# Kernel optimization log

Hardware: AMD Instinct MI355X
Metric: run time of the kernel (lower is better)

The kernel has to match this reference:

```python
import jax, jax.numpy as jnp
import numpy as np

N_ENT = 200000; N_USR = 100000; D = 64
E = 1500000; NI = 1000000
HOPS = 2; N_ITER = 3; N_VIRT = 3; N_REL = 11
EPS = 1e-12


def setup_inputs() -> dict:
    key = jax.random.key(0)
    ks = jax.random.split(key, 8)
    entity_emb = jax.random.normal(ks[0], (N_ENT, D), jnp.float32) * 0.1
    user_emb = jax.random.normal(ks[1], (N_USR, D), jnp.float32) * 0.1
    latent_emb = jax.random.normal(ks[2], (N_VIRT, D), jnp.float32)
    rel_weight = jax.random.normal(ks[3], (N_REL - 1, D), jnp.float32)
    # per-hop Aggregator.w, initialized as in the module
    agg_w = jnp.tile(jnp.array([0.4, 0.3, 0.3], jnp.float32), (HOPS, 1))
    edge_index = jax.random.randint(ks[4], (2, E), 0, N_ENT)
    edge_type = jax.random.randint(ks[5], (E,), 1, N_REL)  # values in [1, n_relations-1]
    user_index = jax.random.randint(ks[6], (NI,), 0, N_USR)
    item_index = jax.random.randint(ks[7], (NI,), 0, N_ENT)
    return dict(entity_emb=entity_emb, user_emb=user_emb, latent_emb=latent_emb,
                rel_weight=rel_weight, agg_w=agg_w, edge_index=edge_index,
                edge_type=edge_type, user_index=user_index, item_index=item_index)


def _l2norm(x):
    n = jnp.linalg.norm(x, axis=1, keepdims=True)
    return x / jnp.maximum(n, EPS)


def _squash(u):
    sq = jnp.sum(u * u, axis=1, keepdims=True)  # ||u||^2
    return (sq / (sq + 1.0)) * _l2norm(u)


def _lws_entity(entity_emb, head, tail, mask_f):
    """LWS over a single virtual-relation edge subset (mask_f zeroes other edges).
    Matches torch: neigh is cumulatively sim-scaled across iterations."""
    cnt = jax.ops.segment_sum(mask_f, head, num_segments=N_ENT)
    denom = jnp.maximum(cnt, 1.0)[:, None]
    neigh = entity_emb[tail] * mask_f[:, None]          # [E, D]
    u = None
    for it in range(N_ITER):
        if u is not None:
            sim = jnp.sum(u[head] * neigh, axis=1, keepdims=True)
            neigh = sim * neigh
        u = jax.ops.segment_sum(neigh, head, num_segments=N_ENT) / denom
        if it < N_ITER - 1:
            u = _squash(u)
        u = u + entity_emb
    return u


def _lws_user(entity_emb, user_emb, user_index, item_index):
    """LWS for users; neigh is re-gathered fresh each iteration (as in torch)."""
    ones = jnp.ones((item_index.shape[0],), entity_emb.dtype)
    cnt = jax.ops.segment_sum(ones, user_index, num_segments=N_USR)
    denom = jnp.maximum(cnt, 1.0)[:, None]
    u = None
    for it in range(N_ITER):
        neigh = entity_emb[item_index]                  # [NI, D]
        if u is not None:
            sim = jnp.sum(u[user_index] * neigh, axis=1, keepdims=True)
            neigh = sim * neigh
        u = jax.ops.segment_sum(neigh, user_index, num_segments=N_USR) / denom
        if it < N_ITER - 1:
            u = _squash(u)
        u = u + user_emb
    return u


def reference(entity_emb, user_emb, latent_emb, rel_weight, agg_w,
              edge_index, edge_type, user_index, item_index):
    head, tail = edge_index[0], edge_index[1]
    # relation -> virtual-relation routing (argmax over similarity)
    relation_remap = jnp.argmax(rel_weight @ latent_emb.T, axis=1)   # [n_rel-1]
    et = relation_remap[edge_type - 1]                               # [E] in [0, N_VIRT)

    entity_res = entity_emb
    user_res = user_emb
    ent = entity_emb
    usr = user_emb
    for hop in range(HOPS):
        items = [_lws_entity(ent, head, tail, (et == i).astype(ent.dtype))
                 for i in range(N_VIRT)]
        w = jax.nn.softmax(agg_w[hop])                               # [3]
        entity_agg = w[0] * items[0] + w[1] * items[1] + w[2] * items[2]
        user_agg = _lws_user(ent, usr, user_index, item_index)
        # no dropout (eval mode); normalize + residual
        ent = _l2norm(entity_agg)
        usr = _l2norm(user_agg)
        entity_res = entity_res + ent
        user_res = user_res + usr
    return jnp.concatenate([entity_res, user_res], axis=0)          # [N_ENT+N_USR, D]
```

## Files before the change

### kernel.cpp

```cpp
#include <hip/hip_runtime.h>

#define N_ENT 200000
#define N_USR 100000
#define NT3   700000
#define UKEY0 600000
#define DIM 64
#define NE 1500000
#define NI_ 1000000
#define NTE 2500000
#define NREL1 10
#define NVIRT 3
#define EPSF 1e-12f
#define SCAN_B 1024
#define RE 6
#define RU 12

__device__ __forceinline__ float4 f4_zero() { return make_float4(0.f, 0.f, 0.f, 0.f); }
__device__ __forceinline__ float4 f4_add(float4 a, float4 b) {
    return make_float4(a.x + b.x, a.y + b.y, a.z + b.z, a.w + b.w);
}
__device__ __forceinline__ float4 f4_scale(float s, float4 a) {
    return make_float4(s * a.x, s * a.y, s * a.z, s * a.w);
}
__device__ __forceinline__ float4 f4_fma(float s, float4 a, float4 b) {
    return make_float4(fmaf(s, a.x, b.x), fmaf(s, a.y, b.y), fmaf(s, a.z, b.z), fmaf(s, a.w, b.w));
}
__device__ __forceinline__ float f4_dot(float4 a, float4 b) {
    return a.x * b.x + a.y * b.y + a.z * b.z + a.w * b.w;
}

__device__ __forceinline__ float red16(float v) {
    int x;
    x = __builtin_amdgcn_update_dpp(0, __float_as_int(v), 0xB1, 0xF, 0xF, true);
    v += __int_as_float(x);
    x = __builtin_amdgcn_update_dpp(0, __float_as_int(v), 0x4E, 0xF, 0xF, true);
    v += __int_as_float(x);
    x = __builtin_amdgcn_update_dpp(0, __float_as_int(v), 0x124, 0xF, 0xF, true);
    v += __int_as_float(x);
    x = __builtin_amdgcn_update_dpp(0, __float_as_int(v), 0x128, 0xF, 0xF, true);
    v += __int_as_float(x);
    return v;
}

__device__ __forceinline__ float4 squash4(float4 u, float sq) {
    float n = sqrtf(sq);
    float s = sq / ((sq + 1.f) * fmaxf(n, EPSF));
    return f4_scale(s, u);
}

__global__ void k_prep(const float* __restrict__ rw, const float* __restrict__ lat,
                       const float* __restrict__ aw, int* __restrict__ remap,
                       float* __restrict__ wsoft) {
    int t = threadIdx.x;
    if (t < NREL1) {
        float best = -3.4e38f; int bi = 0;
        for (int j = 0; j < NVIRT; j++) {
            float s = 0.f;
            for (int d = 0; d < DIM; d++) s += rw[t * DIM + d] * lat[j * DIM + d];
            if (s > best) { best = s; bi = j; }
        }
        remap[t] = bi;
    }
    if (t >= 32 && t < 34) {
        int h = t - 32;
        float a0 = aw[h * 3 + 0], a1 = aw[h * 3 + 1], a2 = aw[h * 3 + 2];
        float m = fmaxf(a0, fmaxf(a1, a2));
        float e0 = expf(a0 - m), e1 = expf(a1 - m), e2 = expf(a2 - m);
        float s = e0 + e1 + e2;
        wsoft[h * 3 + 0] = e0 / s; wsoft[h * 3 + 1] = e1 / s; wsoft[h * 3 + 2] = e2 / s;
    }
}

__global__ void k_count_all(const int* __restrict__ head, const int* __restrict__ etype,
                            const int* __restrict__ remap, const int* __restrict__ uidx,
                            int* __restrict__ cnt) {
    int i = blockIdx.x * blockDim.x + threadIdx.x;
    if (i < NE) {
        int key = head[i] * 3 + remap[etype[i] - 1];
        atomicAdd(&cnt[key], 1);
    } else if (i < NTE) {
        atomicAdd(&cnt[UKEY0 + uidx[i - NE]], 1);
    }
}

__global__ void k_scan1(const int* __restrict__ in, int* __restrict__ excl,
                        int* __restrict__ bsum, int n) {
    __shared__ int s[SCAN_B];
    int tid = threadIdx.x, gid = blockIdx.x * SCAN_B + tid;
    int v = (gid < n) ? in[gid] : 0;
    s[tid] = v; __syncthreads();
    for (int off = 1; off < SCAN_B; off <<= 1) {
        int t = 0;
        if (tid >= off) t = s[tid - off];
        __syncthreads();
        s[tid] += t;
        __syncthreads();
    }
    if (gid < n) excl[gid] = s[tid] - v;
    if (tid == SCAN_B - 1) bsum[blockIdx.x] = s[tid];
}

__global__ void k_scan2(int* __restrict__ bsum, int nb) {
    __shared__ int s[SCAN_B];
    int tid = threadIdx.x;
    int v = (tid < nb) ? bsum[tid] : 0;
    s[tid] = v; __syncthreads();
    for (int off = 1; off < SCAN_B; off <<= 1) {
        int t = 0;
        if (tid >= off) t = s[tid - off];
        __syncthreads();
        s[tid] += t;
        __syncthreads();
    }
    if (tid < nb) bsum[tid] = s[tid] - v;
}

__global__ void k_scan3(const int* __restrict__ excl, const int* __restrict__ bsum,
                        const int* __restrict__ cnt, int* __restrict__ rp,
                        int* __restrict__ cur, int n) {
    int gid = blockIdx.x * SCAN_B + threadIdx.x;
    if (gid < n) {
        int v = excl[gid] + bsum[blockIdx.x];
        rp[gid] = v;
        cur[gid] = v;
        if (gid == n - 1) rp[n] = v + cnt[gid];
    }
}

__global__ void k_scatter_all(const int* __restrict__ head, const int* __restrict__ tail,
                              const int* __restrict__ etype, const int* __restrict__ remap,
                              const int* __restrict__ uidx, const int* __restrict__ iidx,
                              int* __restrict__ cur, int* __restrict__ sorted) {
    int i = blockIdx.x * blockDim.x + threadIdx.x;
    if (i < NE) {
        int key = head[i] * 3 + remap[etype[i] - 1];
        int pos = atomicAdd(&cur[key], 1);
        sorted[pos] = tail[i];
    } else if (i < NTE) {
        int j = i - NE;
        int pos = atomicAdd(&cur[UKEY0 + uidx[j]], 1);
        sorted[pos] = iidx[j];
    }
}

#define NBLK_E (N_ENT / 16)
#define NBLK_U (N_USR / 16)

__global__ __launch_bounds__(256, 5) void k_hop(
    const float* __restrict__ ent, const float* __restrict__ usr,
    const int* __restrict__ rp, const int* __restrict__ sorted,
    const float* __restrict__ wsoft, int hop,
    float* __restrict__ ent_next, float* __restrict__ usr_next,
    int do_store, int first,
    float* __restrict__ outE, float* __restrict__ outU)
{
    int lane = threadIdx.x & 15;
    const float4* entv = (const float4*)ent;

    if (blockIdx.x < NBLK_E) {
        int g = blockIdx.x * 16 + (threadIdx.x >> 4);
        float4 eh = entv[g * 16 + lane];
        float4 agg = f4_zero();

        for (int v = 0; v < NVIRT; v++) {
            int s = rp[g * 3 + v], e = rp[g * 3 + v + 1];
            int deg = e - s;
            float inv = 1.f / fmaxf((float)deg, 1.f);
            int myp = (lane < deg) ? sorted[s + lane] : 0;

            float4 xc[RE];
            float4 acc = f4_zero();
            #pragma unroll
            for (int r = 0; r < RE; r++) {
                if (r < deg) {
                    int p = __shfl(myp, r, 16);
                    float4 x = entv[p * 16 + lane];
                    xc[r] = x;
                    acc = f4_add(acc, x);
                }
            }
            for (int r = RE; r < deg; r++) {
                int p = (r < 16) ? __shfl(myp, r, 16) : sorted[s + r];
                acc = f4_add(acc, entv[p * 16 + lane]);
            }
            float4 u = f4_scale(inv, acc);
            float sq = red16(f4_dot(u, u));
            float4 u1 = f4_add(squash4(u, sq), eh);

            float4 acc1 = f4_zero();
            float d1c[RE];
            float d1me = 0.f;
            #pragma unroll
            for (int r = 0; r < RE; r++) {
                if (r < deg) {
                    float4 x = xc[r];
                    float d1 = red16(f4_dot(u1, x));
                    d1c[r] = d1;
                    acc1 = f4_fma(d1, x, acc1);
                }
            }
            for (int r = RE; r < deg; r++) {
                int p = (r < 16) ? __shfl(myp, r, 16) : sorted[s + r];
                float4 x = entv[p * 16 + lane];
                float d1 = red16(f4_dot(u1, x));
                if (lane == r) d1me = d1;
                acc1 = f4_fma(d1, x, acc1);
            }
            u = f4_scale(inv, acc1);
            sq = red16(f4_dot(u, u));
            float4 u2 = f4_add(squash4(u, sq), eh);

            float4 acc2 = f4_zero();
            #pragma unroll
            for (int r = 0; r < RE; r++) {
                if (r < deg) {
                    float4 x = xc[r];
                    float d2 = red16(f4_dot(u2, x));
                    float d1 = d1c[r];
                    acc2 = f4_fma(d1 * d1 * d2, x, acc2);
                }
            }
            for (int r = RE; r < deg; r++) {
                int p = (r < 16) ? __shfl(myp, r, 16) : sorted[s + r];
                float4 x = entv[p * 16 + lane];
                float d2 = red16(f4_dot(u2, x));
                float d1 = (r < 16) ? __shfl(d1me, r, 16) : red16(f4_dot(u1, x));
                acc2 = f4_fma(d1 * d1 * d2, x, acc2);
            }
            float w = wsoft[hop * 3 + v];
            agg = f4_fma(w * inv, acc2, agg);
        }
        agg = f4_add(agg, eh);
        float sq = red16(f4_dot(agg, agg));
        float nn = sqrtf(sq);
        float4 en = f4_scale(1.f / fmaxf(nn, EPSF), agg);
        if (do_store) ((float4*)ent_next)[g * 16 + lane] = en;
        float4* outv = (float4*)outE;
        float4 base = first ? eh : outv[g * 16 + lane];
        outv[g * 16 + lane] = f4_add(base, en);
    } else {
        int gu = (blockIdx.x - NBLK_E) * 16 + (threadIdx.x >> 4);
        int s = rp[UKEY0 + gu], e = rp[UKEY0 + gu + 1];
        int deg = e - s;
        const float4* usrv = (const float4*)usr;
        float4 uh = usrv[gu * 16 + lane];
        float inv = 1.f / fmaxf((float)deg, 1.f);

        int deg16 = (deg < 16) ? deg : 16;
        int myp = (lane < deg16) ? sorted[s + lane] : 0;

        float4 xc[RU];
        float4 acc = f4_zero();
        #pragma unroll
        for (int r = 0; r < RU; r++) {
            if (r < deg) {
                int p = __shfl(myp, r, 16);
                float4 x = entv[p * 16 + lane];
                xc[r] = x;
                acc = f4_add(acc, x);
            }
        }
        for (int r = RU; r < deg; r++) {
            int p = (r < 16) ? __shfl(myp, r, 16) : sorted[s + r];
            acc = f4_add(acc, entv[p * 16 + lane]);
        }
        float4 u = f4_scale(inv, acc);
        float sq = red16(f4_dot(u, u));
        float4 u1 = f4_add(squash4(u, sq), uh);

        acc = f4_zero();
        #pragma unroll
        for (int r = 0; r < RU; r++) {
            if (r < deg) {
                float4 x = xc[r];
                acc = f4_fma(red16(f4_dot(u1, x)), x, acc);
            }
        }
        for (int r = RU; r < deg; r++) {
            int p = (r < 16) ? __shfl(myp, r, 16) : sorted[s + r];
            float4 x = entv[p * 16 + lane];
            acc = f4_fma(red16(f4_dot(u1, x)), x, acc);
        }
        u = f4_scale(inv, acc);
        sq = red16(f4_dot(u, u));
        float4 u2 = f4_add(squash4(u, sq), uh);

        acc = f4_zero();
        #pragma unroll
        for (int r = 0; r < RU; r++) {
            if (r < deg) {
                float4 x = xc[r];
                acc = f4_fma(red16(f4_dot(u2, x)), x, acc);
            }
        }
        for (int r = RU; r < deg; r++) {
            int p = (r < 16) ? __shfl(myp, r, 16) : sorted[s + r];
            float4 x = entv[p * 16 + lane];
            acc = f4_fma(red16(f4_dot(u2, x)), x, acc);
        }
        float4 u3 = f4_add(f4_scale(inv, acc), uh);
        sq = red16(f4_dot(u3, u3));
        float nn = sqrtf(sq);
        float4 un = f4_scale(1.f / fmaxf(nn, EPSF), u3);
        if (do_store) ((float4*)usr_next)[gu * 16 + lane] = un;
        float4* outv = (float4*)outU;
        float4 base = first ? uh : outv[gu * 16 + lane];
        outv[gu * 16 + lane] = f4_add(base, un);
    }
}

extern "C" void kernel_launch(void* const* d_in, const int* in_sizes, int n_in,
                              void* d_out, int out_size, void* d_ws, size_t ws_size,
                              hipStream_t stream)
{
    const float* entity_emb = (const float*)d_in[0];
    const float* user_emb   = (const float*)d_in[1];
    const float* latent     = (const float*)d_in[2];
    const float* rel_w      = (const float*)d_in[3];
    const float* agg_w      = (const float*)d_in[4];
    const int* edge_index   = (const int*)d_in[5];
    const int* edge_type    = (const int*)d_in[6];
    const int* user_index   = (const int*)d_in[7];
    const int* item_index   = (const int*)d_in[8];
    float* out = (float*)d_out;

    char* ws = (char*)d_ws;
    size_t off = 0;
    auto alloc = [&](size_t bytes) -> void* {
        void* p = ws + off;
        off += (bytes + 255) / 256 * 256;
        return p;
    };
    float* entA  = (float*)alloc((size_t)N_ENT * DIM * 4);
    float* usrA  = (float*)alloc((size_t)N_USR * DIM * 4);
    float* wsoft = (float*)alloc(8 * 4);
    int* remap   = (int*)alloc(16 * 4);
    int* cnt     = (int*)alloc((size_t)NT3 * 4);
    int* rp      = (int*)alloc((size_t)(NT3 + 1) * 4);
    int* cur     = (int*)alloc((size_t)NT3 * 4);
    int* excl    = (int*)alloc((size_t)NT3 * 4);
    int* bsum    = (int*)alloc(1024 * 4);
    int* sorted  = (int*)alloc((size_t)NTE * 4);

    const int* head = edge_index;
    const int* tail = edge_index + NE;

    hipMemsetAsync(cnt, 0, (size_t)NT3 * 4, stream);

    k_prep<<<1, 64, 0, stream>>>(rel_w, latent, agg_w, remap, wsoft);

    k_count_all<<<(NTE + 255) / 256, 256, 0, stream>>>(head, edge_type, remap, user_index, cnt);

    int nb = (NT3 + SCAN_B - 1) / SCAN_B;
    k_scan1<<<nb, SCAN_B, 0, stream>>>(cnt, excl, bsum, NT3);
    k_scan2<<<1, SCAN_B, 0, stream>>>(bsum, nb);
    k_scan3<<<nb, SCAN_B, 0, stream>>>(excl, bsum, cnt, rp, cur, NT3);

    k_scatter_all<<<(NTE + 255) / 256, 256, 0, stream>>>(
        head, tail, edge_type, remap, user_index, item_index, cur, sorted);

    const float* ec = entity_emb;
    const float* uc = user_emb;
    for (int hop = 0; hop < 2; hop++) {
        int do_store = (hop == 0);
        int first = (hop == 0);
        k_hop<<<NBLK_E + NBLK_U, 256, 0, stream>>>(
            ec, uc, rp, sorted, wsoft, hop, entA, usrA, do_store, first,
            out, out + (size_t)N_ENT * DIM);
        ec = entA;
        uc = usrA;
    }
}
```

Measured before the change: 784.4 us.

## Interleave three virtual-relation LWS passes per entity to overlap gathers

New measurement: 1.091 ms. 1.39x slower.

```diff
diff --git a/kernel.cpp b/kernel.cpp
--- a/kernel.cpp
+++ b/kernel.cpp
@@ -146,7 +146,7 @@
 #define NBLK_E (N_ENT / 16)
 #define NBLK_U (N_USR / 16)
 
-__global__ __launch_bounds__(256, 5) void k_hop(
+__global__ __launch_bounds__(256, 3) void k_hop(
     const float* __restrict__ ent, const float* __restrict__ usr,
     const int* __restrict__ rp, const int* __restrict__ sorted,
     const float* __restrict__ wsoft, int hop,
@@ -160,75 +160,95 @@
     if (blockIdx.x < NBLK_E) {
         int g = blockIdx.x * 16 + (threadIdx.x >> 4);
         float4 eh = entv[g * 16 + lane];
-        float4 agg = f4_zero();
-
-        for (int v = 0; v < NVIRT; v++) {
-            int s = rp[g * 3 + v], e = rp[g * 3 + v + 1];
-            int deg = e - s;
-            float inv = 1.f / fmaxf((float)deg, 1.f);
-            int myp = (lane < deg) ? sorted[s + lane] : 0;
-
-            float4 xc[RE];
-            float4 acc = f4_zero();
+
+        int b3 = g * 3;
+        int q0 = rp[b3], q1 = rp[b3 + 1], q2 = rp[b3 + 2], q3 = rp[b3 + 3];
+        int sA[3] = {q0, q1, q2};
+        int dA[3] = {q1 - q0, q2 - q1, q3 - q2};
+        float invA[3];
+
+        float4 xc[3][RE];
+        float  d1c[3][RE];
+        float4 u1v[3], u2v[3];
+
+        float4 acc0[3];
+        #pragma unroll
+        for (int v = 0; v < 3; v++) {
+            int s = sA[v], deg = dA[v];
+            invA[v] = 1.f / fmaxf((float)deg, 1.f);
+            float4 a = f4_zero();
             #pragma unroll
             for (int r = 0; r < RE; r++) {
                 if (r < deg) {
-                    int p = __shfl(myp, r, 16);
+                    int p = sorted[s + r];
                     float4 x = entv[p * 16 + lane];
-                    xc[r] = x;
-                    acc = f4_add(acc, x);
+                    xc[v][r] = x;
+                    a = f4_add(a, x);
                 }
             }
             for (int r = RE; r < deg; r++) {
-                int p = (r < 16) ? __shfl(myp, r, 16) : sorted[s + r];
-                acc = f4_add(acc, entv[p * 16 + lane]);
-            }
-            float4 u = f4_scale(inv, acc);
+                int p = sorted[s + r];
+                a = f4_add(a, entv[p * 16 + lane]);
+            }
+            acc0[v] = a;
+        }
+        #pragma unroll
+        for (int v = 0; v < 3; v++) {
+            float4 u = f4_scale(invA[v], acc0[v]);
             float sq = red16(f4_dot(u, u));
-            float4 u1 = f4_add(squash4(u, sq), eh);
-
-            float4 acc1 = f4_zero();
-            float d1c[RE];
-            float d1me = 0.f;
+            u1v[v] = f4_add(squash4(u, sq), eh);
+        }
+        float4 acc1[3];
+        #pragma unroll
+        for (int v = 0; v < 3; v++) {
+            int s = sA[v], deg = dA[v];
+            float4 a = f4_zero();
             #pragma unroll
             for (int r = 0; r < RE; r++) {
                 if (r < deg) {
-                    float4 x = xc[r];
-                    float d1 = red16(f4_dot(u1, x));
-                    d1c[r] = d1;
-                    acc1 = f4_fma(d1, x, acc1);
+                    float4 x = xc[v][r];
+                    float d1 = red16(f4_dot(u1v[v], x));
+                    d1c[v][r] = d1;
+                    a = f4_fma(d1, x, a);
                 }
             }
             for (int r = RE; r < deg; r++) {
-                int p = (r < 16) ? __shfl(myp, r, 16) : sorted[s + r];
+                int p = sorted[s + r];
                 float4 x = entv[p * 16 + lane];
-                float d1 = red16(f4_dot(u1, x));
-                if (lane == r) d1me = d1;
-                acc1 = f4_fma(d1, x, acc1);
-            }
-            u = f4_scale(inv, acc1);
-            sq = red16(f4_dot(u, u));
-            float4 u2 = f4_add(squash4(u, sq), eh);
-
-            float4 acc2 = f4_zero();
+                float d1 = red16(f4_dot(u1v[v], x));
+                a = f4_fma(d1, x, a);
+            }
+            acc1[v] = a;
+        }
+        #pragma unroll
+        for (int v = 0; v < 3; v++) {
+            float4 u = f4_scale(invA[v], acc1[v]);
+            float sq = red16(f4_dot(u, u));
+            u2v[v] = f4_add(squash4(u, sq), eh);
+        }
+        float4 agg = f4_zero();
+        #pragma unroll
+        for (int v = 0; v < 3; v++) {
+            int s = sA[v], deg = dA[v];
+            float4 a = f4_zero();
             #pragma unroll
             for (int r = 0; r < RE; r++) {
                 if (r < deg) {
-                    float4 x = xc[r];
-                    float d2 = red16(f4_dot(u2, x));
-                    float d1 = d1c[r];
-                    acc2 = f4_fma(d1 * d1 * d2, x, acc2);
+                    float4 x = xc[v][r];
+                    float d2 = red16(f4_dot(u2v[v], x));
+                    float d1 = d1c[v][r];
+                    a = f4_fma(d1 * d1 * d2, x, a);
                 }
             }
             for (int r = RE; r < deg; r++) {
-                int p = (r < 16) ? __shfl(myp, r, 16) : sorted[s + r];
+                int p = sorted[s + r];
                 float4 x = entv[p * 16 + lane];
-                float d2 = red16(f4_dot(u2, x));
-                float d1 = (r < 16) ? __shfl(d1me, r, 16) : red16(f4_dot(u1, x));
-                acc2 = f4_fma(d1 * d1 * d2, x, acc2);
+                float d2 = red16(f4_dot(u2v[v], x));
+                float d1 = red16(f4_dot(u1v[v], x));
+                a = f4_fma(d1 * d1 * d2, x, a);
             }
             float w = wsoft[hop * 3 + v];
-            agg = f4_fma(w * inv, acc2, agg);
+            agg = f4_fma(w * invA[v], a, agg);
         }
         agg = f4_add(agg, eh);
         float sq = red16(f4_dot(agg, agg));
@@ -246,22 +266,19 @@
         float4 uh = usrv[gu * 16 + lane];
         float inv = 1.f / fmaxf((float)deg, 1.f);
 
-        int deg16 = (deg < 16) ? deg : 16;
-        int myp = (lane < deg16) ? sorted[s + lane] : 0;
-
         float4 xc[RU];
         float4 acc = f4_zero();
         #pragma unroll
         for (int r = 0; r < RU; r++) {
             if (r < deg) {
-                int p = __shfl(myp, r, 16);
+                int p = sorted[s + r];
                 float4 x = entv[p * 16 + lane];
                 xc[r] = x;
                 acc = f4_add(acc, x);
             }
         }
         for (int r = RU; r < deg; r++) {
-            int p = (r < 16) ? __shfl(myp, r, 16) : sorted[s + r];
+            int p = sorted[s + r];
             acc = f4_add(acc, entv[p * 16 + lane]);
         }
         float4 u = f4_scale(inv, acc);
@@ -277,7 +294,7 @@
             }
         }
         for (int r = RU; r < deg; r++) {
-            int p = (r < 16) ? __shfl(myp, r, 16) : sorted[s + r];
+            int p = sorted[s + r];
             float4 x = entv[p * 16 + lane];
             acc = f4_fma(red16(f4_dot(u1, x)), x, acc);
         }
@@ -294,7 +311,7 @@
             }
         }
         for (int r = RU; r < deg; r++) {
-            int p = (r < 16) ? __shfl(myp, r, 16) : sorted[s + r];
+            int p = sorted[s + r];
             float4 x = entv[p * 16 + lane];
             acc = f4_fma(red16(f4_dot(u2, x)), x, acc);
         }
```

## Drop prep and scan2 kernels by recomputing remap/softmax per block and fusing scans

Applied to the files above, without the earlier changes.

Result: no change. 771.0 us (-1.7%).

```diff
diff --git a/kernel.cpp b/kernel.cpp
--- a/kernel.cpp
+++ b/kernel.cpp
@@ -48,9 +48,9 @@
     return f4_scale(s, u);
 }
 
-__global__ void k_prep(const float* __restrict__ rw, const float* __restrict__ lat,
-                       const float* __restrict__ aw, int* __restrict__ remap,
-                       float* __restrict__ wsoft) {
+__device__ __forceinline__ void block_remap(const float* __restrict__ rw,
+                                            const float* __restrict__ lat,
+                                            int* sremap) {
     int t = threadIdx.x;
     if (t < NREL1) {
         float best = -3.4e38f; int bi = 0;
@@ -59,24 +59,19 @@
             for (int d = 0; d < DIM; d++) s += rw[t * DIM + d] * lat[j * DIM + d];
             if (s > best) { best = s; bi = j; }
         }
-        remap[t] = bi;
-    }
-    if (t >= 32 && t < 34) {
-        int h = t - 32;
-        float a0 = aw[h * 3 + 0], a1 = aw[h * 3 + 1], a2 = aw[h * 3 + 2];
-        float m = fmaxf(a0, fmaxf(a1, a2));
-        float e0 = expf(a0 - m), e1 = expf(a1 - m), e2 = expf(a2 - m);
-        float s = e0 + e1 + e2;
-        wsoft[h * 3 + 0] = e0 / s; wsoft[h * 3 + 1] = e1 / s; wsoft[h * 3 + 2] = e2 / s;
-    }
+        sremap[t] = bi;
+    }
+    __syncthreads();
 }
 
 __global__ void k_count_all(const int* __restrict__ head, const int* __restrict__ etype,
-                            const int* __restrict__ remap, const int* __restrict__ uidx,
-                            int* __restrict__ cnt) {
+                            const float* __restrict__ rw, const float* __restrict__ lat,
+                            const int* __restrict__ uidx, int* __restrict__ cnt) {
+    __shared__ int sremap[NREL1];
+    block_remap(rw, lat, sremap);
     int i = blockIdx.x * blockDim.x + threadIdx.x;
     if (i < NE) {
-        int key = head[i] * 3 + remap[etype[i] - 1];
+        int key = head[i] * 3 + sremap[etype[i] - 1];
         atomicAdd(&cnt[key], 1);
     } else if (i < NTE) {
         atomicAdd(&cnt[UKEY0 + uidx[i - NE]], 1);
@@ -100,40 +95,38 @@
     if (tid == SCAN_B - 1) bsum[blockIdx.x] = s[tid];
 }
 
-__global__ void k_scan2(int* __restrict__ bsum, int nb) {
+__global__ void k_scan23(const int* __restrict__ excl, const int* __restrict__ bsum,
+                         const int* __restrict__ cnt, int* __restrict__ rp,
+                         int* __restrict__ cur, int n, int nb) {
     __shared__ int s[SCAN_B];
     int tid = threadIdx.x;
-    int v = (tid < nb) ? bsum[tid] : 0;
-    s[tid] = v; __syncthreads();
-    for (int off = 1; off < SCAN_B; off <<= 1) {
-        int t = 0;
-        if (tid >= off) t = s[tid - off];
+    int v = (tid < nb && tid < (int)blockIdx.x) ? bsum[tid] : 0;
+    s[tid] = v;
+    __syncthreads();
+    for (int off = SCAN_B / 2; off > 0; off >>= 1) {
+        if (tid < off) s[tid] += s[tid + off];
         __syncthreads();
-        s[tid] += t;
-        __syncthreads();
-    }
-    if (tid < nb) bsum[tid] = s[tid] - v;
-}
-
-__global__ void k_scan3(const int* __restrict__ excl, const int* __restrict__ bsum,
-                        const int* __restrict__ cnt, int* __restrict__ rp,
-                        int* __restrict__ cur, int n) {
-    int gid = blockIdx.x * SCAN_B + threadIdx.x;
+    }
+    int prefix = s[0];
+    int gid = blockIdx.x * SCAN_B + tid;
     if (gid < n) {
-        int v = excl[gid] + bsum[blockIdx.x];
-        rp[gid] = v;
-        cur[gid] = v;
-        if (gid == n - 1) rp[n] = v + cnt[gid];
+        int val = excl[gid] + prefix;
+        rp[gid] = val;
+        cur[gid] = val;
+        if (gid == n - 1) rp[n] = val + cnt[gid];
     }
 }
 
 __global__ void k_scatter_all(const int* __restrict__ head, const int* __restrict__ tail,
-                              const int* __restrict__ etype, const int* __restrict__ remap,
+                              const int* __restrict__ etype,
+                              const float* __restrict__ rw, const float* __restrict__ lat,
                               const int* __restrict__ uidx, const int* __restrict__ iidx,
                               int* __restrict__ cur, int* __restrict__ sorted) {
+    __shared__ int sremap[NREL1];
+    block_remap(rw, lat, sremap);
     int i = blockIdx.x * blockDim.x + threadIdx.x;
     if (i < NE) {
-        int key = head[i] * 3 + remap[etype[i] - 1];
+        int key = head[i] * 3 + sremap[etype[i] - 1];
         int pos = atomicAdd(&cur[key], 1);
         sorted[pos] = tail[i];
     } else if (i < NTE) {
@@ -149,7 +142,7 @@
 __global__ __launch_bounds__(256, 5) void k_hop(
     const float* __restrict__ ent, const float* __restrict__ usr,
     const int* __restrict__ rp, const int* __restrict__ sorted,
-    const float* __restrict__ wsoft, int hop,
+    const float* __restrict__ aw, int hop,
     float* __restrict__ ent_next, float* __restrict__ usr_next,
     int do_store, int first,
     float* __restrict__ outE, float* __restrict__ outU)
@@ -162,11 +155,26 @@
         float4 eh = entv[g * 16 + lane];
         float4 agg = f4_zero();
 
+        float a0 = aw[hop * 3 + 0], a1 = aw[hop * 3 + 1], a2 = aw[hop * 3 + 2];
+        float m = fmaxf(a0, fmaxf(a1, a2));
+        float e0 = expf(a0 - m), e1 = expf(a1 - m), e2 = expf(a2 - m);
+        float esum = e0 + e1 + e2;
+        float w0 = e0 / esum, w1 = e1 / esum, w2 = e2 / esum;
+
+        int b3 = g * 3;
+        int s0 = rp[b3], s1 = rp[b3 + 1], s2 = rp[b3 + 2], s3 = rp[b3 + 3];
+        int dg0 = s1 - s0, dg1 = s2 - s1, dg2 = s3 - s2;
+        int myp0 = (lane < dg0) ? sorted[s0 + lane] : 0;
+        int myp1 = (lane < dg1) ? sorted[s1 + lane] : 0;
+        int myp2 = (lane < dg2) ? sorted[s2 + lane] : 0;
+
+        #pragma unroll
         for (int v = 0; v < NVIRT; v++) {
-            int s = rp[g * 3 + v], e = rp[g * 3 + v + 1];
-            int deg = e - s;
+            int s   = (v == 0) ? s0   : (v == 1) ? s1   : s2;
+            int deg = (v == 0) ? dg0  : (v == 1) ? dg1  : dg2;
+            int myp = (v == 0) ? myp0 : (v == 1) ? myp1 : myp2;
+            float w = (v == 0) ? w0   : (v == 1) ? w1   : w2;
             float inv = 1.f / fmaxf((float)deg, 1.f);
-            int myp = (lane < deg) ? sorted[s + lane] : 0;
 
             float4 xc[RE];
             float4 acc = f4_zero();
@@ -227,7 +235,6 @@
                 float d1 = (r < 16) ? __shfl(d1me, r, 16) : red16(f4_dot(u1, x));
                 acc2 = f4_fma(d1 * d1 * d2, x, acc2);
             }
-            float w = wsoft[hop * 3 + v];
             agg = f4_fma(w * inv, acc2, agg);
         }
         agg = f4_add(agg, eh);
@@ -333,8 +340,6 @@
     };
     float* entA  = (float*)alloc((size_t)N_ENT * DIM * 4);
     float* usrA  = (float*)alloc((size_t)N_USR * DIM * 4);
-    float* wsoft = (float*)alloc(8 * 4);
-    int* remap   = (int*)alloc(16 * 4);
     int* cnt     = (int*)alloc((size_t)NT3 * 4);
     int* rp      = (int*)alloc((size_t)(NT3 + 1) * 4);
     int* cur     = (int*)alloc((size_t)NT3 * 4);
@@ -347,17 +352,15 @@
 
     hipMemsetAsync(cnt, 0, (size_t)NT3 * 4, stream);
 
-    k_prep<<<1, 64, 0, stream>>>(rel_w, latent, agg_w, remap, wsoft);
-
-    k_count_all<<<(NTE + 255) / 256, 256, 0, stream>>>(head, edge_type, remap, user_index, cnt);
+    k_count_all<<<(NTE + 255) / 256, 256, 0, stream>>>(
+        head, edge_type, rel_w, latent, user_index, cnt);
 
     int nb = (NT3 + SCAN_B - 1) / SCAN_B;
     k_scan1<<<nb, SCAN_B, 0, stream>>>(cnt, excl, bsum, NT3);
-    k_scan2<<<1, SCAN_B, 0, stream>>>(bsum, nb);
-    k_scan3<<<nb, SCAN_B, 0, stream>>>(excl, bsum, cnt, rp, cur, NT3);
+    k_scan23<<<nb, SCAN_B, 0, stream>>>(excl, bsum, cnt, rp, cur, NT3, nb);
 
     k_scatter_all<<<(NTE + 255) / 256, 256, 0, stream>>>(
-        head, tail, edge_type, remap, user_index, item_index, cur, sorted);
+        head, tail, edge_type, rel_w, latent, user_index, item_index, cur, sorted);
 
     const float* ec = entity_emb;
     const float* uc = user_emb;
@@ -365,7 +368,7 @@
         int do_store = (hop == 0);
         int first = (hop == 0);
         k_hop<<<NBLK_E + NBLK_U, 256, 0, stream>>>(
-            ec, uc, rp, sorted, wsoft, hop, entA, usrA, do_store, first,
+            ec, uc, rp, sorted, agg_w, hop, entA, usrA, do_store, first,
             out, out + (size_t)N_ENT * DIM);
         ec = entA;
         uc = usrA;
```
